# Kernel tuning notes

Hardware: AMD Instinct MI355X
Metric: run time of the kernel (lower is better)

Reference implementation:

```python
import jax, jax.numpy as jnp
import numpy as np

TAU = 2.0        # spikingjelly LIFNode default tau
VTH = 1.0        # v_threshold
ALPHA = 2.0      # ATan surrogate default alpha
NWIN = (4, 4, 4)
TOPK = 4
HEADS = 8

@jax.custom_vjp
def spike(x):
    return (x >= 0.0).astype(x.dtype)

def _spike_fwd(x):
    return spike(x), x

def _spike_bwd(x, g):
    # ATan surrogate: d/dx ~ alpha/2 / (1 + (pi/2 * alpha * x)^2)
    s = (jnp.pi / 2) * ALPHA * x
    return (g * (ALPHA / 2) / (1 + s * s),)

spike.defvjp(_spike_fwd, _spike_bwd)

def lif(x):
    # fresh-state single-step LIF: H = x/tau, spike if H >= v_threshold
    return spike(x / TAU - VTH)

def setup_inputs() -> dict:
    key = jax.random.key(0)
    ks = jax.random.split(key, 4)
    T, B, Lt, Lh, Lw, C = 4, 2, 8, 32, 32, 256
    x = jax.random.normal(ks[0], (T, B, Lt, Lh, Lw, C), jnp.float32)
    W_qkv = jax.random.normal(ks[1], (C, 3 * C), jnp.float32) / np.sqrt(C)
    b_qkv = jnp.zeros((3 * C,), jnp.float32)
    W_proj = jax.random.normal(ks[2], (C, C), jnp.float32) / np.sqrt(C)
    b_proj = jnp.zeros((C,), jnp.float32)
    return {"x": x, "W_qkv": W_qkv, "b_qkv": b_qkv, "W_proj": W_proj, "b_proj": b_proj}

def reference(x, W_qkv, b_qkv, W_proj, b_proj):
    T, B, Lt, Lh, Lw, C = x.shape
    wt, wh, ww = NWIN
    H = HEADS
    hd = C // H
    nw = wt * wh * ww
    pt, ph, pw = Lt // wt, Lh // wh, Lw // ww
    ws = pt * ph * pw

    # windowize: [T,B,nw,ws,C]
    xw = x.reshape(T, B, wt, pt, wh, ph, ww, pw, C)
    xw = xw.transpose(0, 1, 2, 4, 6, 3, 5, 7, 8).reshape(T, B, nw, ws, C)

    # region-level routing scores over windows
    region = xw.sum(0).mean(2)                                  # [B,nw,C]
    scores = jnp.einsum('bic,bjc->bij', region, region) * (hd ** -0.5)
    idx = jax.lax.top_k(scores, TOPK)[1]                        # [B,nw,topk]

    qkv = xw @ W_qkv + b_qkv                                    # [T,B,nw,ws,3C]
    q, k, v = jnp.split(qkv, 3, axis=-1)
    q, k, v = lif(q), lif(k), lif(v)
    q = q.reshape(T, B, nw, ws, H, hd)
    k = k.reshape(T, B, nw, ws, H, hd)
    v = v.reshape(T, B, nw, ws, H, hd)

    # per-batch gather of topk routed windows' k/v
    gather = jax.vmap(lambda kb, ib: kb[:, ib], in_axes=(1, 0), out_axes=1)
    k_g = gather(k, idx).reshape(T, B, nw, TOPK * ws, H, hd)    # [T,B,nw,topk*ws,H,hd]
    v_g = gather(v, idx).reshape(T, B, nw, TOPK * ws, H, hd)

    # linear (kernelized) attention: kv = k^T v, out = q kv / (q sum_k)
    kv = jnp.einsum('tbnshd,tbnshe->tbnhde', k_g, v_g)          # [T,B,nw,H,hd,hd]
    out = jnp.einsum('tbnshd,tbnhde->tbnshe', q, kv)            # [T,B,nw,ws,H,hd]
    ksum = k_g.sum(3)                                           # [T,B,nw,H,hd]
    D = jnp.einsum('tbnshd,tbnhd->tbnsh', q, ksum)[..., None]   # [T,B,nw,ws,H,1]
    out = out / (D + 1e-6)

    out = out.reshape(T, B, nw, ws, C) @ W_proj + b_proj

    # un-windowize
    out = out.reshape(T, B, wt, wh, ww, pt, ph, pw, C)
    out = out.transpose(0, 1, 2, 5, 3, 6, 4, 7, 8).reshape(T, B, Lt, Lh, Lw, C)
    return out
```

## Files before the change

kernel.cpp:

```cpp
#include <hip/hip_runtime.h>
#include <cstdint>
#include <cstddef>

#define T_    4
#define B_    2
#define NW_   64
#define WS_   128
#define C_    256
#define NC3   768
#define H_    8
#define HD_   32
#define TOPK_ 4
#define RCAP  131072
#define BAND  0.008f
#define RBCAP 512

#define OFF_A2     0ull
#define OFF_BQ     67108864ull
#define OFF_BP     67502080ull
#define OFF_QM     67895296ull
#define OFF_KB     69992448ull
#define OFF_VB     72089600ull
#define OFF_KV     74186752ull
#define OFF_PART   91488256ull
#define OFF_REGION 92012544ull
#define OFF_IDX    92143616ull
#define OFF_RL     92145664ull
#define OFF_RC     92669952ull

typedef short short8 __attribute__((ext_vector_type(8)));
typedef float floatx4 __attribute__((ext_vector_type(4)));

__device__ __forceinline__ short f2bf(float f) {
    unsigned u = __float_as_uint(f);
    unsigned r = (u + 0x7fffu + ((u >> 16) & 1u)) >> 16;
    return (short)r;
}
__device__ __forceinline__ float bf2f(short h) {
    return __uint_as_float(((unsigned)(unsigned short)h) << 16);
}

__device__ __forceinline__ void gload_lds16(const void* g, void* l) {
    __builtin_amdgcn_global_load_lds(
        (const __attribute__((address_space(1))) unsigned*)g,
        (__attribute__((address_space(3))) unsigned*)l,
        16, 0, 0);
}

__device__ __forceinline__ int xoff_row(int g, int s) {
    int tb = g >> 6;
    int n  = g & 63;
    int iwt = n >> 4, iwh = (n >> 2) & 3, iww = n & 3;
    int ipt = s >> 6, iph = (s >> 3) & 7, ipw = s & 7;
    int lt = iwt * 2 + ipt, lh = iwh * 8 + iph, lw = iww * 8 + ipw;
    return (((tb * 8 + lt) * 32 + lh) * 32 + lw) * 256;
}

__global__ __launch_bounds__(256) void k_prep(const float* __restrict__ x,
        const float* __restrict__ Wqkv, const float* __restrict__ Wp,
        float* __restrict__ part, short* __restrict__ A2,
        short* __restrict__ Bq, short* __restrict__ Bp) {
    const int bid = blockIdx.x;
    const int tid = threadIdx.x;
    if (bid < 512) {
        int g = bid;
        int c = tid;
        const int ktAh = c >> 5, ktAl = 8 + (c >> 5);
        const int octsh = ((c >> 3) & 3) << 4, sub = c & 7;
        float acc = 0.f;
        for (int s = 0; s < WS_; ++s) {
            float v = x[xoff_row(g, s) + c];
            acc += v;
            short hi = f2bf(v);
            short lo = f2bf(v - bf2f(hi));
            int lane = (s & 15) | octsh;
            size_t base = ((size_t)(g * 8 + (s >> 4))) * 16;
            A2[(base + ktAh) * 512 + lane * 8 + sub] = hi;
            A2[(base + ktAl) * 512 + lane * 8 + sub] = lo;
        }
        part[g * C_ + c] = acc;
    } else if (bid < 1280) {
        int u = bid - 512;
        int ke = u & 255;
        int n = (u >> 8) * 256 + tid;
        float wv = Wqkv[(size_t)ke * NC3 + n];
        short o = f2bf(wv);
        int gj = n >> 4, lmn = n & 15, ktB = ke >> 5, oct = (ke >> 3) & 3, sub = ke & 7;
        Bq[(size_t)((gj * 8 + ktB) * 64 + (lmn | (oct << 4))) * 8 + sub] = o;
    } else {
        int ke = bid - 1280;
        int n = tid;
        float wv = Wp[(size_t)(ke & 255) * 256 + n];
        short hi = f2bf(wv);
        short o = (ke < 512) ? hi : f2bf(wv - bf2f(hi));
        int gj = n >> 4, lmn = n & 15, ktB = ke >> 5, oct = (ke >> 3) & 3, sub = ke & 7;
        Bp[(size_t)((gj * 24 + ktB) * 64 + (lmn | (oct << 4))) * 8 + sub] = o;
    }
}

__global__ __launch_bounds__(256) void k_region(const float* __restrict__ part,
                                                float* __restrict__ region) {
    int bn = blockIdx.x;
    int c = threadIdx.x;
    int b = bn >> 6, n = bn & 63;
    float acc = 0.f;
    for (int t = 0; t < T_; ++t) acc += part[((t * 2 + b) * 64 + n) * C_ + c];
    region[bn * C_ + c] = acc * (1.0f / 128.0f);
}

__global__ __launch_bounds__(64) void k_scores(const float* __restrict__ region,
                                               int* __restrict__ idx) {
    int bi = blockIdx.x;
    int b = bi >> 6, i = bi & 63;
    int tid = threadIdx.x;
    __shared__ float ri[C_];
    __shared__ float sc[64];
    for (int c = tid; c < C_; c += 64) ri[c] = region[(b * 64 + i) * C_ + c];
    __syncthreads();
    const float* rj = region + (size_t)(b * 64 + tid) * C_;
    float dot = 0.f;
    for (int c = 0; c < C_; ++c) dot += ri[c] * rj[c];
    sc[tid] = dot * 0.17677669529663687f;
    __syncthreads();
    if (tid == 0) {
        for (int kk = 0; kk < TOPK_; ++kk) {
            float best = -INFINITY; int bj = 0;
            for (int j = 0; j < 64; ++j)
                if (sc[j] > best) { best = sc[j]; bj = j; }
            idx[bi * TOPK_ + kk] = bj;
            sc[bj] = -INFINITY;
        }
    }
}

__device__ __forceinline__ unsigned p4(unsigned xv) {
    return (xv & 1u) | ((xv >> 7) & 2u) | ((xv >> 14) & 4u) | ((xv >> 21) & 8u);
}

__global__ __launch_bounds__(256, 2) void qkv_mfma(const short* __restrict__ A2,
        const short* __restrict__ Bq, const float* __restrict__ bias,
        unsigned* __restrict__ qm, unsigned* __restrict__ kb,
        unsigned* __restrict__ vb, unsigned* __restrict__ rl,
        unsigned* __restrict__ rcnt) {
    __shared__ __align__(16) char stg[2][32768];
    __shared__ unsigned rbuf[RBCAP];
    __shared__ unsigned lcnt, sbase;
    const int bid = blockIdx.x;
    const int x8 = bid & 7;
    const int y = bid >> 3;
    const int p = y % 3;
    const int mb = x8 + ((y / 3) << 3);
    const int tid = threadIdx.x;
    const int wv = tid >> 6, lane = tid & 63;
    const int wm = wv >> 1, wn = wv & 1;
    const int lm = lane & 15, lq = lane >> 4;

    if (tid == 0) lcnt = 0;

    const char* Ag = (const char*)(A2 + (size_t)mb * 65536);
    const char* Bg = (const char*)(Bq + (size_t)p * 65536);
    const int laneoff = lane * 16;

#define STAGE_CHUNK(buf, ktB_)                                                 \
    {                                                                          \
        _Pragma("unroll")                                                      \
        for (int k = 0; k < 4; ++k) {                                          \
            int slot = k * 4 + wv;                                             \
            int gi = slot >> 1, hl = slot & 1;                                 \
            const char* src = Ag + (((gi * 16) + (ktB_) + hl * 8) << 10) + laneoff; \
            gload_lds16(src, &stg[buf][k * 4096 + wv * 1024 + laneoff]);       \
        }                                                                      \
        _Pragma("unroll")                                                      \
        for (int k = 0; k < 4; ++k) {                                          \
            int slot = k * 4 + wv;                                             \
            const char* src = Bg + ((slot * 8 + (ktB_)) << 10) + laneoff;      \
            gload_lds16(src, &stg[buf][16384 + k * 4096 + wv * 1024 + laneoff]); \
        }                                                                      \
    }

    floatx4 acc[4][8];
#pragma unroll
    for (int i = 0; i < 4; ++i)
#pragma unroll
        for (int j = 0; j < 8; ++j) acc[i][j] = (floatx4)0.f;

    STAGE_CHUNK(0, 0);
    __syncthreads();

    for (int ktB = 0; ktB < 8; ++ktB) {
        int cur = ktB & 1;
        if (ktB < 7) STAGE_CHUNK(cur ^ 1, ktB + 1);
        const char* sb = &stg[cur][0];
        short8 ah[4], al[4], bf[8];
#pragma unroll
        for (int j = 0; j < 8; ++j)
            bf[j] = *(const short8*)(sb + 16384 + ((wn * 8 + j) << 10) + laneoff);
#pragma unroll
        for (int i = 0; i < 4; ++i) {
            ah[i] = *(const short8*)(sb + (((wm * 4 + i) * 2 + 0) << 10) + laneoff);
            al[i] = *(const short8*)(sb + (((wm * 4 + i) * 2 + 1) << 10) + laneoff);
        }
#pragma unroll
        for (int i = 0; i < 4; ++i)
#pragma unroll
            for (int j = 0; j < 8; ++j)
                acc[i][j] = __builtin_amdgcn_mfma_f32_16x16x32_bf16(
                    ah[i], bf[j], acc[i][j], 0, 0, 0);
#pragma unroll
        for (int i = 0; i < 4; ++i)
#pragma unroll
            for (int j = 0; j < 8; ++j)
                acc[i][j] = __builtin_amdgcn_mfma_f32_16x16x32_bf16(
                    al[i], bf[j], acc[i][j], 0, 0, 0);
        __syncthreads();
    }

    unsigned char* sp = (unsigned char*)&stg[0][0];
#pragma unroll
    for (int i = 0; i < 4; ++i) {
#pragma unroll
        for (int j = 0; j < 8; ++j) {
            int cb = wn * 128 + j * 16 + lm;
            int cg = p * 256 + cb;
            float bj = bias[cg];
#pragma unroll
            for (int r = 0; r < 4; ++r) {
                int s = wm * 64 + i * 16 + lq * 4 + r;
                float v = acc[i][j][r] + bj;
                if (fabsf(v - 2.0f) < BAND) {
                    unsigned ent = ((unsigned)mb << 17) | ((unsigned)s << 10) | (unsigned)cg;
                    unsigned slot = atomicAdd(&lcnt, 1u);
                    if (slot < RBCAP) {
                        rbuf[slot] = ent;
                    } else {
                        unsigned gs = atomicAdd(rcnt, 1u);
                        if (gs < RCAP) rl[gs] = ent;
                    }
                }
                sp[s * 264 + cb] = (v >= 2.0f) ? 1 : 0;
            }
        }
    }
    __syncthreads();

    unsigned cnt = lcnt;
    if (cnt > RBCAP) cnt = RBCAP;
    if (tid == 0) sbase = atomicAdd(rcnt, cnt);
    __syncthreads();
    for (unsigned e = tid; e < cnt; e += 256) {
        unsigned slot = sbase + e;
        if (slot < RCAP) rl[slot] = rbuf[e];
    }

    if (p == 0) {
        const unsigned* spw = (const unsigned*)sp;
#pragma unroll
        for (int t = 0; t < 4; ++t) {
            int w = t * 256 + tid;
            int s = w >> 3, h = w & 7;
            unsigned m = 0;
#pragma unroll
            for (int q = 0; q < 8; ++q)
                m |= p4(spw[s * 66 + h * 8 + q]) << (q * 4);
            qm[(size_t)mb * 1024 + w] = m;
        }
    } else {
        unsigned wrd[4];
#pragma unroll
        for (int w2 = 0; w2 < 4; ++w2) {
            unsigned m = 0;
#pragma unroll
            for (int ii = 0; ii < 32; ++ii)
                m |= (unsigned)(sp[(w2 * 32 + ii) * 264 + tid] & 1) << ii;
            wrd[w2] = m;
        }
        uint4 o; o.x = wrd[0]; o.y = wrd[1]; o.z = wrd[2]; o.w = wrd[3];
        *(uint4*)(((p == 1) ? kb : vb) + ((size_t)mb * 256 + tid) * 4) = o;
    }
}

__global__ __launch_bounds__(256) void rescue_fix(const float* __restrict__ x,
        const float* __restrict__ W, const float* __restrict__ bias,
        const unsigned* __restrict__ rl, const unsigned* __restrict__ rcnt,
        unsigned* __restrict__ qm, unsigned* __restrict__ kb,
        unsigned* __restrict__ vb) {
    unsigned n = *rcnt; if (n > RCAP) n = RCAP;
    unsigned gid = blockIdx.x * 256 + threadIdx.x;
    unsigned stride = gridDim.x * 256;
    for (unsigned e = gid; e < n; e += stride) {
        unsigned ent = rl[e];
        int mb = ent >> 17, s = (ent >> 10) & 127, cg = ent & 1023;
        const float* ar = x + xoff_row(mb, s);
        const float* wc = W + cg;
        float da = 0.f;
#pragma unroll 4
        for (int k4 = 0; k4 < 64; ++k4) {
            float4 a4 = *(const float4*)(ar + k4 * 4);
            da = fmaf(a4.x, wc[(size_t)(k4 * 4 + 0) * NC3], da);
            da = fmaf(a4.y, wc[(size_t)(k4 * 4 + 1) * NC3], da);
            da = fmaf(a4.z, wc[(size_t)(k4 * 4 + 2) * NC3], da);
            da = fmaf(a4.w, wc[(size_t)(k4 * 4 + 3) * NC3], da);
        }
        da += bias[cg];
        int spk = (da >= 2.0f) ? 1 : 0;
        if (cg < 256) {
            int h = cg >> 5, d = cg & 31;
            unsigned* wp = qm + (size_t)mb * 1024 + s * 8 + h;
            unsigned bit = 1u << d;
            int have = (*wp & bit) ? 1 : 0;
            if (have != spk) atomicXor(wp, bit);
        } else {
            unsigned* tgt = (cg < 512) ? kb : vb;
            int c = cg & 255;
            unsigned* wp = tgt + ((size_t)mb * 256 + c) * 4 + (s >> 5);
            unsigned bit = 1u << (s & 31);
            int have = (*wp & bit) ? 1 : 0;
            if (have != spk) atomicXor(wp, bit);
        }
    }
}

__global__ __launch_bounds__(256) void kv_bits(const unsigned* __restrict__ kb,
        const unsigned* __restrict__ vb, const int* __restrict__ idx,
        unsigned short* __restrict__ kvbuf) {
    int g = blockIdx.x;
    int tb = g >> 6, n = g & 63, b = tb & 1;
    int tid = threadIdx.x;
    __shared__ uint4 kbl[1024];
    __shared__ uint4 vbl[1024];
    __shared__ int widx[TOPK_];
    if (tid < TOPK_) widx[tid] = idx[(b * 64 + n) * TOPK_ + tid];
    __syncthreads();
#pragma unroll
    for (int kk = 0; kk < TOPK_; ++kk) {
        int g2 = tb * 64 + widx[kk];
        kbl[kk * 256 + tid] = *(const uint4*)&kb[((size_t)g2 * 256 + tid) * 4];
        vbl[kk * 256 + tid] = *(const uint4*)&vb[((size_t)g2 * 256 + tid) * 4];
    }
    __syncthreads();
    int h = tid >> 5, e = tid & 31;
    uint4 vw0 = vbl[0 * 256 + h * 32 + e];
    uint4 vw1 = vbl[1 * 256 + h * 32 + e];
    uint4 vw2 = vbl[2 * 256 + h * 32 + e];
    uint4 vw3 = vbl[3 * 256 + h * 32 + e];
    for (int d = 0; d < 32; ++d) {
        uint4 k0 = kbl[0 * 256 + h * 32 + d];
        uint4 k1 = kbl[1 * 256 + h * 32 + d];
        uint4 k2 = kbl[2 * 256 + h * 32 + d];
        uint4 k3 = kbl[3 * 256 + h * 32 + d];
        int acc = __popc(k0.x & vw0.x) + __popc(k0.y & vw0.y)
                + __popc(k0.z & vw0.z) + __popc(k0.w & vw0.w)
                + __popc(k1.x & vw1.x) + __popc(k1.y & vw1.y)
                + __popc(k1.z & vw1.z) + __popc(k1.w & vw1.w)
                + __popc(k2.x & vw2.x) + __popc(k2.y & vw2.y)
                + __popc(k2.z & vw2.z) + __popc(k2.w & vw2.w)
                + __popc(k3.x & vw3.x) + __popc(k3.y & vw3.y)
                + __popc(k3.z & vw3.z) + __popc(k3.w & vw3.w);
        kvbuf[((size_t)(g * 8 + h) * 32 + d) * 32 + e] = (unsigned short)acc;
    }
}

__global__ __launch_bounds__(256) void attn_proj(const unsigned* __restrict__ qm,
        const unsigned short* __restrict__ kvbuf, const unsigned* __restrict__ kb,
        const int* __restrict__ idx, const short* __restrict__ Bp,
        const float* __restrict__ bias, float* __restrict__ out) {
    __shared__ __align__(16) short aw[16384];
    __shared__ unsigned qb[256];
    __shared__ float ksl[256];
    __shared__ int widx[TOPK_];
    const int bid = blockIdx.x;
    const int g = bid >> 2, qr = bid & 3;
    const int tb = g >> 6, n = g & 63, b = tb & 1;
    const int tid = threadIdx.x;
    if (tid < TOPK_) widx[tid] = idx[(b * 64 + n) * TOPK_ + tid];
    __syncthreads();
    float ks = 0.f;
#pragma unroll
    for (int kk = 0; kk < TOPK_; ++kk) {
        uint4 kw = *(const uint4*)&kb[((size_t)(tb * 64 + widx[kk]) * 256 + tid) * 4];
        ks += (float)(__popc(kw.x) + __popc(kw.y) + __popc(kw.z) + __popc(kw.w));
    }
    ksl[tid] = ks;
    qb[tid] = qm[(size_t)g * 1024 + qr * 256 + tid];
    __syncthreads();

    const int h = tid >> 5, e = tid & 31;
    float kvr[32], ksr[32];
#pragma unroll
    for (int d = 0; d < 32; ++d)
        kvr[d] = (float)kvbuf[((size_t)(g * 8 + h) * 32 + d) * 32 + e];
#pragma unroll
    for (int d = 0; d < 32; ++d) ksr[d] = ksl[h * 32 + d];

    const int ktAh = tid >> 5, ktAl = 8 + (tid >> 5);
    const int octsh = ((tid >> 3) & 3) << 4, sub = tid & 7;
    for (int sl = 0; sl < 32; ++sl) {
        unsigned qw = qb[sl * 8 + h];
        float r;
        if (qw == 0u) {
            r = 0.f;
        } else {
            float num = 0.f, den = 0.f;
#pragma unroll
            for (int by = 0; by < 4; ++by) {
                unsigned byt = (qw >> (by * 8)) & 0xffu;
                if (byt) {
#pragma unroll
                    for (int dd = 0; dd < 8; ++dd) {
                        float m = (float)((byt >> dd) & 1u);
                        num = fmaf(m, kvr[by * 8 + dd], num);
                        den = fmaf(m, ksr[by * 8 + dd], den);
                    }
                }
            }
            r = num / (den + 1e-6f);
        }
        short hi = f2bf(r), lo = f2bf(r - bf2f(hi));
        int lane2 = (sl & 15) | octsh;
        int gi = sl >> 4;
        aw[((gi * 16 + ktAh) * 64 + lane2) * 8 + sub] = hi;
        aw[((gi * 16 + ktAl) * 64 + lane2) * 8 + sub] = lo;
    }
    __syncthreads();

    const int wvw = tid >> 6, lane = tid & 63;
    const int lm = lane & 15, lq = lane >> 4;
    floatx4 pacc[2][4];
#pragma unroll
    for (int i = 0; i < 2; ++i)
#pragma unroll
        for (int j = 0; j < 4; ++j) pacc[i][j] = (floatx4)0.f;
    const short* Bb = Bp + ((size_t)(wvw * 4) * 24) * 512 + lane * 8;
#pragma unroll 2
    for (int kt = 0; kt < 24; ++kt) {
        int ktA = (kt < 16) ? kt : kt - 16;
        short8 af[2], bf[4];
#pragma unroll
        for (int i = 0; i < 2; ++i)
            af[i] = *(const short8*)&aw[((i * 16 + ktA) * 64 + lane) * 8];
#pragma unroll
        for (int j = 0; j < 4; ++j)
            bf[j] = *(const short8*)(Bb + (size_t)(j * 24 + kt) * 512);
#pragma unroll
        for (int i = 0; i < 2; ++i)
#pragma unroll
            for (int j = 0; j < 4; ++j)
                pacc[i][j] = __builtin_amdgcn_mfma_f32_16x16x32_bf16(
                    af[i], bf[j], pacc[i][j], 0, 0, 0);
    }
    __syncthreads();

    float* ow = (float*)aw;
#pragma unroll
    for (int i = 0; i < 2; ++i) {
#pragma unroll
        for (int j = 0; j < 4; ++j) {
            int c = wvw * 64 + j * 16 + lm;
            float bj = bias[c];
#pragma unroll
            for (int r = 0; r < 4; ++r)
                ow[(i * 16 + lq * 4 + r) * 256 + c] = pacc[i][j][r] + bj;
        }
    }
    __syncthreads();

    int sl2 = tid >> 3, pc = (tid & 7) * 32;
    int off = xoff_row(g, qr * 32 + sl2) + pc;
#pragma unroll
    for (int q = 0; q < 8; ++q)
        *(float4*)(out + off + q * 4) = *(const float4*)&ow[sl2 * 256 + pc + q * 4];
}

extern "C" void kernel_launch(void* const* d_in, const int* in_sizes, int n_in,
                              void* d_out, int out_size, void* d_ws, size_t ws_size,
                              hipStream_t stream) {
    (void)in_sizes; (void)n_in; (void)out_size; (void)ws_size;
    const float* x    = (const float*)d_in[0];
    const float* Wqkv = (const float*)d_in[1];
    const float* bqkv = (const float*)d_in[2];
    const float* Wp   = (const float*)d_in[3];
    const float* bp   = (const float*)d_in[4];
    char* ws = (char*)d_ws;
    short*    A2    = (short*)   (ws + OFF_A2);
    short*    Bq    = (short*)   (ws + OFF_BQ);
    short*    Bpj   = (short*)   (ws + OFF_BP);
    unsigned* qmv   = (unsigned*)(ws + OFF_QM);
    unsigned* kb    = (unsigned*)(ws + OFF_KB);
    unsigned* vb    = (unsigned*)(ws + OFF_VB);
    unsigned short* kvbuf = (unsigned short*)(ws + OFF_KV);
    float*    part  = (float*)   (ws + OFF_PART);
    float*    region= (float*)   (ws + OFF_REGION);
    int*      idxb  = (int*)     (ws + OFF_IDX);
    unsigned* rl    = (unsigned*)(ws + OFF_RL);
    unsigned* rcnt  = (unsigned*)(ws + OFF_RC);
    float*    out   = (float*)d_out;

    hipMemsetAsync(rcnt, 0, 4, stream);
    k_prep     <<<2048, 256, 0, stream>>>(x, Wqkv, Wp, part, A2, Bq, Bpj);
    k_region   <<<128, 256, 0, stream>>>(part, region);
    k_scores   <<<128,  64, 0, stream>>>(region, idxb);
    qkv_mfma   <<<1536, 256, 0, stream>>>(A2, Bq, bqkv, qmv, kb, vb, rl, rcnt);
    rescue_fix <<<256, 256, 0, stream>>>(x, Wqkv, bqkv, rl, rcnt, qmv, kb, vb);
    kv_bits    <<<512, 256, 0, stream>>>(kb, vb, idxb, kvbuf);
    attn_proj  <<<2048, 256, 0, stream>>>(qmv, kvbuf, kb, idxb, Bpj, bp, out);
}
```

Baseline: 230.9 us.

## Compute q·kv numerator with bf16 MFMA using split hi/lo kv fragments

kv_bits now writes the kv counts as split bf16 hi/lo values, laid out directly as MFMA B-fragments. attn_proj replaces the per-thread scalar bit-masked FMA loop over 32 dims with 16x16x32 bf16 MFMAs, using spike bits expanded to bf16 1.0 as the A operand. The denominator is computed separately into shared memory. This removes the serial 32-step per-thread scalar loop and the 32 register-held kv values, at the cost of twice the MFMA work for the hi/lo split and a small extra shared buffer with a sync.

```diff
diff --git a/kernel.cpp b/kernel.cpp
--- a/kernel.cpp
+++ b/kernel.cpp
@@ -322,7 +322,7 @@
 
 __global__ __launch_bounds__(256) void kv_bits(const unsigned* __restrict__ kb,
         const unsigned* __restrict__ vb, const int* __restrict__ idx,
-        unsigned short* __restrict__ kvbuf) {
+        short* __restrict__ kvf) {
     int g = blockIdx.x;
     int tb = g >> 6, n = g & 63, b = tb & 1;
     int tid = threadIdx.x;
@@ -339,34 +339,48 @@
     }
     __syncthreads();
     int h = tid >> 5, e = tid & 31;
+    int ei = e >> 4;
     uint4 vw0 = vbl[0 * 256 + h * 32 + e];
     uint4 vw1 = vbl[1 * 256 + h * 32 + e];
     uint4 vw2 = vbl[2 * 256 + h * 32 + e];
     uint4 vw3 = vbl[3 * 256 + h * 32 + e];
-    for (int d = 0; d < 32; ++d) {
-        uint4 k0 = kbl[0 * 256 + h * 32 + d];
-        uint4 k1 = kbl[1 * 256 + h * 32 + d];
-        uint4 k2 = kbl[2 * 256 + h * 32 + d];
-        uint4 k3 = kbl[3 * 256 + h * 32 + d];
-        int acc = __popc(k0.x & vw0.x) + __popc(k0.y & vw0.y)
-                + __popc(k0.z & vw0.z) + __popc(k0.w & vw0.w)
-                + __popc(k1.x & vw1.x) + __popc(k1.y & vw1.y)
-                + __popc(k1.z & vw1.z) + __popc(k1.w & vw1.w)
-                + __popc(k2.x & vw2.x) + __popc(k2.y & vw2.y)
-                + __popc(k2.z & vw2.z) + __popc(k2.w & vw2.w)
-                + __popc(k3.x & vw3.x) + __popc(k3.y & vw3.y)
-                + __popc(k3.z & vw3.z) + __popc(k3.w & vw3.w);
-        kvbuf[((size_t)(g * 8 + h) * 32 + d) * 32 + e] = (unsigned short)acc;
+#pragma unroll
+    for (int oct = 0; oct < 4; ++oct) {
+        short8 hi8, lo8;
+#pragma unroll
+        for (int dd = 0; dd < 8; ++dd) {
+            int d = oct * 8 + dd;
+            uint4 k0 = kbl[0 * 256 + h * 32 + d];
+            uint4 k1 = kbl[1 * 256 + h * 32 + d];
+            uint4 k2 = kbl[2 * 256 + h * 32 + d];
+            uint4 k3 = kbl[3 * 256 + h * 32 + d];
+            int acc = __popc(k0.x & vw0.x) + __popc(k0.y & vw0.y)
+                    + __popc(k0.z & vw0.z) + __popc(k0.w & vw0.w)
+                    + __popc(k1.x & vw1.x) + __popc(k1.y & vw1.y)
+                    + __popc(k1.z & vw1.z) + __popc(k1.w & vw1.w)
+                    + __popc(k2.x & vw2.x) + __popc(k2.y & vw2.y)
+                    + __popc(k2.z & vw2.z) + __popc(k2.w & vw2.w)
+                    + __popc(k3.x & vw3.x) + __popc(k3.y & vw3.y)
+                    + __popc(k3.z & vw3.z) + __popc(k3.w & vw3.w);
+            float v = (float)acc;
+            short hv = f2bf(v);
+            hi8[dd] = hv;
+            lo8[dd] = f2bf(v - bf2f(hv));
+        }
+        int ln = (e & 15) | (oct << 4);
+        *(short8*)&kvf[((((size_t)g * 8 + h) * 2 + 0) * 2 + ei) * 512 + ln * 8] = hi8;
+        *(short8*)&kvf[((((size_t)g * 8 + h) * 2 + 1) * 2 + ei) * 512 + ln * 8] = lo8;
     }
 }
 
 __global__ __launch_bounds__(256) void attn_proj(const unsigned* __restrict__ qm,
-        const unsigned short* __restrict__ kvbuf, const unsigned* __restrict__ kb,
+        const short* __restrict__ kvf, const unsigned* __restrict__ kb,
         const int* __restrict__ idx, const short* __restrict__ Bp,
         const float* __restrict__ bias, float* __restrict__ out) {
     __shared__ __align__(16) short aw[16384];
     __shared__ unsigned qb[256];
     __shared__ float ksl[256];
+    __shared__ float denl[256];
     __shared__ int widx[TOPK_];
     const int bid = blockIdx.x;
     const int g = bid >> 2, qr = bid & 3;
@@ -384,46 +398,79 @@
     qb[tid] = qm[(size_t)g * 1024 + qr * 256 + tid];
     __syncthreads();
 
-    const int h = tid >> 5, e = tid & 31;
-    float kvr[32], ksr[32];
-#pragma unroll
-    for (int d = 0; d < 32; ++d)
-        kvr[d] = (float)kvbuf[((size_t)(g * 8 + h) * 32 + d) * 32 + e];
-#pragma unroll
-    for (int d = 0; d < 32; ++d) ksr[d] = ksl[h * 32 + d];
-
-    const int ktAh = tid >> 5, ktAl = 8 + (tid >> 5);
-    const int octsh = ((tid >> 3) & 3) << 4, sub = tid & 7;
-    for (int sl = 0; sl < 32; ++sl) {
+    {
+        int h = tid >> 5, sl = tid & 31;
         unsigned qw = qb[sl * 8 + h];
-        float r;
-        if (qw == 0u) {
-            r = 0.f;
-        } else {
-            float num = 0.f, den = 0.f;
-#pragma unroll
-            for (int by = 0; by < 4; ++by) {
-                unsigned byt = (qw >> (by * 8)) & 0xffu;
-                if (byt) {
-#pragma unroll
-                    for (int dd = 0; dd < 8; ++dd) {
-                        float m = (float)((byt >> dd) & 1u);
-                        num = fmaf(m, kvr[by * 8 + dd], num);
-                        den = fmaf(m, ksr[by * 8 + dd], den);
-                    }
+        float den = 0.f;
+#pragma unroll
+        for (int d = 0; d < 32; ++d)
+            den += ((qw >> d) & 1u) ? ksl[h * 32 + d] : 0.f;
+        denl[tid] = den;
+    }
+    __syncthreads();
+
+    const int wvw = tid >> 6, lane = tid & 63;
+    const int oct = lane >> 4, l15 = lane & 15;
+
+    floatx4 nacc[2][2][2];
+#pragma unroll
+    for (int h2 = 0; h2 < 2; ++h2)
+#pragma unroll
+        for (int mi = 0; mi < 2; ++mi)
+#pragma unroll
+            for (int ei = 0; ei < 2; ++ei) nacc[h2][mi][ei] = (floatx4)0.f;
+
+#pragma unroll
+    for (int h2 = 0; h2 < 2; ++h2) {
+        int h = wvw * 2 + h2;
+        short8 a0, a1;
+        {
+            unsigned byt = (qb[(l15)*8 + h] >> (oct * 8)) & 0xffu;
+#pragma unroll
+            for (int j = 0; j < 8; ++j)
+                a0[j] = ((byt >> j) & 1u) ? (short)0x3F80 : (short)0;
+        }
+        {
+            unsigned byt = (qb[(16 + l15)*8 + h] >> (oct * 8)) & 0xffu;
+#pragma unroll
+            for (int j = 0; j < 8; ++j)
+                a1[j] = ((byt >> j) & 1u) ? (short)0x3F80 : (short)0;
+        }
+#pragma unroll
+        for (int ei = 0; ei < 2; ++ei) {
+            short8 bh = *(const short8*)&kvf[((((size_t)g * 8 + h) * 2 + 0) * 2 + ei) * 512 + lane * 8];
+            short8 bl = *(const short8*)&kvf[((((size_t)g * 8 + h) * 2 + 1) * 2 + ei) * 512 + lane * 8];
+            nacc[h2][0][ei] = __builtin_amdgcn_mfma_f32_16x16x32_bf16(a0, bh, nacc[h2][0][ei], 0, 0, 0);
+            nacc[h2][0][ei] = __builtin_amdgcn_mfma_f32_16x16x32_bf16(a0, bl, nacc[h2][0][ei], 0, 0, 0);
+            nacc[h2][1][ei] = __builtin_amdgcn_mfma_f32_16x16x32_bf16(a1, bh, nacc[h2][1][ei], 0, 0, 0);
+            nacc[h2][1][ei] = __builtin_amdgcn_mfma_f32_16x16x32_bf16(a1, bl, nacc[h2][1][ei], 0, 0, 0);
+        }
+    }
+
+#pragma unroll
+    for (int h2 = 0; h2 < 2; ++h2) {
+        int h = wvw * 2 + h2;
+#pragma unroll
+        for (int mi = 0; mi < 2; ++mi) {
+#pragma unroll
+            for (int ei = 0; ei < 2; ++ei) {
+                int e = ei * 16 + l15;
+                int lane2base = (((e >> 3) & 3) << 4);
+                int sub = e & 7;
+#pragma unroll
+                for (int r = 0; r < 4; ++r) {
+                    int sl = mi * 16 + oct * 4 + r;
+                    float rv = nacc[h2][mi][ei][r] / (denl[h * 32 + sl] + 1e-6f);
+                    short hi = f2bf(rv), lo = f2bf(rv - bf2f(hi));
+                    int lane2 = (sl & 15) | lane2base;
+                    aw[((mi * 16 + h) * 64 + lane2) * 8 + sub] = hi;
+                    aw[((mi * 16 + 8 + h) * 64 + lane2) * 8 + sub] = lo;
                 }
             }
-            r = num / (den + 1e-6f);
-        }
-        short hi = f2bf(r), lo = f2bf(r - bf2f(hi));
-        int lane2 = (sl & 15) | octsh;
-        int gi = sl >> 4;
-        aw[((gi * 16 + ktAh) * 64 + lane2) * 8 + sub] = hi;
-        aw[((gi * 16 + ktAl) * 64 + lane2) * 8 + sub] = lo;
-    }
-    __syncthreads();
-
-    const int wvw = tid >> 6, lane = tid & 63;
+        }
+    }
+    __syncthreads();
+
     const int lm = lane & 15, lq = lane >> 4;
     floatx4 pacc[2][4];
 #pragma unroll
@@ -487,7 +534,7 @@
     unsigned* qmv   = (unsigned*)(ws + OFF_QM);
     unsigned* kb    = (unsigned*)(ws + OFF_KB);
     unsigned* vb    = (unsigned*)(ws + OFF_VB);
-    unsigned short* kvbuf = (unsigned short*)(ws + OFF_KV);
+    short*    kvf   = (short*)   (ws + OFF_KV);
     float*    part  = (float*)   (ws + OFF_PART);
     float*    region= (float*)   (ws + OFF_REGION);
     int*      idxb  = (int*)     (ws + OFF_IDX);
@@ -501,6 +548,6 @@
     k_scores   <<<128,  64, 0, stream>>>(region, idxb);
     qkv_mfma   <<<1536, 256, 0, stream>>>(A2, Bq, bqkv, qmv, kb, vb, rl, rcnt);
     rescue_fix <<<256, 256, 0, stream>>>(x, Wqkv, bqkv, rl, rcnt, qmv, kb, vb);
-    kv_bits    <<<512, 256, 0, stream>>>(kb, vb, idxb, kvbuf);
-    attn_proj  <<<2048, 256, 0, stream>>>(qmv, kvbuf, kb, idxb, Bpj, bp, out);
-}
+    kv_bits    <<<512, 256, 0, stream>>>(kb, vb, idxb, kvf);
+    attn_proj  <<<2048, 256, 0, stream>>>(qmv, kvf, kb, idxb, Bpj, bp, out);
+}
```

New measurement: 217.1 us, median of 3. 1.06x faster.
